# Kernel tuning notes

Measured on AMD Instinct MI355X. Metric: run time of the kernel, lower is better.

Reference implementation:

```python
import jax, jax.numpy as jnp
import numpy as np

B, S, HID = 2, 2048, 4096
H, KV, D = 32, 8, 128
ROPE_BASE = 10000.0
SCALE = 1.0 / (D ** 0.5)


def setup_inputs() -> dict:
    key = jax.random.key(0)
    k1, k2, k3 = jax.random.split(key, 3)
    hidden_states = jax.random.normal(k1, (B, S, HID), dtype=jnp.float32)
    position_ids = jnp.broadcast_to(jnp.arange(S, dtype=jnp.int32)[None, :], (B, S))
    Wqkv = jax.random.normal(k2, ((H + 2 * KV) * D, HID), dtype=jnp.float32) * (HID ** -0.5)
    Wo = jax.random.normal(k3, (HID, HID), dtype=jnp.float32) * (HID ** -0.5)
    return {"hidden_states": hidden_states, "position_ids": position_ids,
            "Wqkv": Wqkv, "Wo": Wo}


def _rotate_half(x):
    x1, x2 = jnp.split(x, 2, axis=-1)
    return jnp.concatenate([-x2, x1], axis=-1)


def _rope_cos_sin(position_ids):
    # inv_freq: [D/2]
    inv_freq = 1.0 / (ROPE_BASE ** (jnp.arange(0, D, 2, dtype=jnp.float32) / D))
    freqs = position_ids.astype(jnp.float32)[:, :, None] * inv_freq[None, None, :]  # [B,S,D/2]
    emb = jnp.concatenate([freqs, freqs], axis=-1)  # [B,S,D]
    # broadcast over heads: [B,1,S,D]
    return jnp.cos(emb)[:, None, :, :], jnp.sin(emb)[:, None, :, :]


def reference(hidden_states, position_ids, Wqkv, Wo):
    # fused QKV projection (no bias)
    qkv = jnp.einsum('bsh,oh->bso', hidden_states, Wqkv)  # [B,S,(H+2KV)*D]
    q, k, v = jnp.split(qkv, [H * D, (H + KV) * D], axis=-1)
    q = q.reshape(B, S, H, D).transpose(0, 2, 1, 3)    # [B,H,S,D]
    k = k.reshape(B, S, KV, D).transpose(0, 2, 1, 3)   # [B,KV,S,D]
    v = v.reshape(B, S, KV, D).transpose(0, 2, 1, 3)   # [B,KV,S,D]

    cos, sin = _rope_cos_sin(position_ids)
    q = q * cos + _rotate_half(q) * sin
    k = k * cos + _rotate_half(k) * sin

    # GQA: repeat_interleave kv heads to match q heads
    rep = H // KV
    k_full = jnp.repeat(k, rep, axis=1)  # [B,H,S,D]
    v_full = jnp.repeat(v, rep, axis=1)

    scores = jnp.einsum('bhqd,bhkd->bhqk', q, k_full) * SCALE  # [B,H,S,S]
    causal = jnp.tril(jnp.ones((S, S), dtype=bool))
    scores = jnp.where(causal[None, None, :, :], scores, jnp.float32(-jnp.inf))
    attn = jax.nn.softmax(scores, axis=-1)
    out = jnp.einsum('bhqk,bhkd->bhqd', attn, v_full)  # [B,H,S,D]
    out = out.transpose(0, 2, 1, 3).reshape(B, S, H * D)
    return jnp.einsum('bso,ho->bsh', out, Wo)  # o_proj, Wo is [out,in]
```

## Files before the change

kernel.cpp:

```cpp
#include <hip/hip_runtime.h>
#include <stdint.h>
#include <stddef.h>

#define Bsz   2
#define Ssz   2048
#define HIDsz 4096
#define Hsz   32
#define KVsz  8
#define Dsz   128
#define NQKV  6144
#define QSCALE 0.12752057463f
#define L2_1E4_64 0.20762050595f

typedef __bf16 bf16x8 __attribute__((ext_vector_type(8)));
typedef __bf16 bf16x2 __attribute__((ext_vector_type(2)));
typedef float  f32x4  __attribute__((ext_vector_type(4)));
typedef float  f32x16 __attribute__((ext_vector_type(16)));
typedef unsigned short u16;
typedef u16 u16x4 __attribute__((ext_vector_type(4)));
typedef u16 u16x8 __attribute__((ext_vector_type(8)));
typedef uint32_t u32x4 __attribute__((ext_vector_type(4)));

__device__ __forceinline__ u16 f2bf(float f) {
  uint32_t u = __builtin_bit_cast(uint32_t, f);
  u = (u + 0x7FFFu + ((u >> 16) & 1u)) >> 16;
  return (u16)u;
}
__device__ __forceinline__ float bf2f(u16 h) {
  return __builtin_bit_cast(float, (uint32_t)h << 16);
}
__device__ __forceinline__ uint32_t packc(float lo, float hi_) {
  bf16x2 t;
  t[0] = (__bf16)lo; t[1] = (__bf16)hi_;
  return __builtin_bit_cast(uint32_t, t);
}

#define GLDS(gp, lp) __builtin_amdgcn_global_load_lds( \
    (__attribute__((address_space(1))) void*)(void*)(gp), \
    (__attribute__((address_space(3))) void*)(lp), 16, 0, 0)

#define N4_HS  ((Bsz * Ssz * HIDsz) / 4)
#define N4_WQ  ((NQKV * HIDsz) / 4)
#define N4_WO  ((HIDsz * HIDsz) / 4)
__global__ __launch_bounds__(256) void k_cvt3(const float* __restrict__ hs,
                                              const float* __restrict__ wqkv,
                                              const float* __restrict__ wo,
                                              u16* __restrict__ xbf,
                                              u16* __restrict__ wqbf,
                                              u16* __restrict__ wobf) {
  int i = blockIdx.x * 256 + threadIdx.x;
  const float* src; u16* dst; int off;
  if (i < N4_HS)                   { src = hs;   dst = xbf;  off = i; }
  else if (i < N4_HS + N4_WQ)      { src = wqkv; dst = wqbf; off = i - N4_HS; }
  else if (i < N4_HS + N4_WQ + N4_WO) { src = wo; dst = wobf; off = i - N4_HS - N4_WQ; }
  else return;
  float4 v = ((const float4*)src)[off];
  u16x4 o;
  o.x = f2bf(v.x); o.y = f2bf(v.y); o.z = f2bf(v.z); o.w = f2bf(v.w);
  ((u16x4*)dst)[off] = o;
}


#define BARX do { asm volatile("" ::: "memory"); __builtin_amdgcn_s_barrier(); \
                  asm volatile("" ::: "memory"); } while (0)
#define VM6  asm volatile("s_waitcnt vmcnt(6)" ::: "memory")
#define VM0  asm volatile("s_waitcnt vmcnt(0)" ::: "memory")

#define LOADA4(P_, Q_, F_) do {                                               \
    afr[F_][0] = LDA(P_, Q_, 0, 0); afr[F_][1] = LDA(P_, Q_, 0, 1);           \
    afr[F_][2] = LDA(P_, Q_, 1, 0); afr[F_][3] = LDA(P_, Q_, 1, 1);           \
  } while (0)

#define LOADB8(P_) do {                                                       \
    _Pragma("unroll") for (int nf = 0; nf < 4; ++nf) {                        \
      bfr[nf][0] = LDB(P_, nf, 0); bfr[nf][1] = LDB(P_, nf, 1); }             \
  } while (0)

#define MMA16(Q_, F_) do {                                                    \
    __builtin_amdgcn_s_setprio(1);                                            \
    _Pragma("unroll") for (int nf = 0; nf < 4; ++nf) {                        \
      acc[(Q_)*2][nf]   = __builtin_amdgcn_mfma_f32_16x16x32_bf16(afr[F_][0], bfr[nf][0], acc[(Q_)*2][nf],   0,0,0); \
      acc[(Q_)*2+1][nf] = __builtin_amdgcn_mfma_f32_16x16x32_bf16(afr[F_][2], bfr[nf][0], acc[(Q_)*2+1][nf], 0,0,0); \
    }                                                                         \
    _Pragma("unroll") for (int nf = 0; nf < 4; ++nf) {                        \
      acc[(Q_)*2][nf]   = __builtin_amdgcn_mfma_f32_16x16x32_bf16(afr[F_][1], bfr[nf][1], acc[(Q_)*2][nf],   0,0,0); \
      acc[(Q_)*2+1][nf] = __builtin_amdgcn_mfma_f32_16x16x32_bf16(afr[F_][3], bfr[nf][1], acc[(Q_)*2+1][nf], 0,0,0); \
    }                                                                         \
    __builtin_amdgcn_s_setprio(0);                                            \
  } while (0)

#define TLS 258

template <int MODE>
__global__ __launch_bounds__(512, 1) void k_gemm256(const u16* __restrict__ A,
                                                    const u16* __restrict__ Bm,
                                                    float* __restrict__ Cv,
                                                    const int* __restrict__ pos,
                                                    u16* __restrict__ Qr,
                                                    int M, int N, int K_ld,
                                                    int K_len) {
  constexpr int LDS_BYTES = (MODE == 1) ? (256 * TLS * 2) : (4 * 256 * 64 * 2);
  __shared__ __align__(16) char LDSBUF[LDS_BYTES];
  u16* SA0 = (u16*)LDSBUF;
  u16* SB0 = (u16*)(LDSBUF + 65536);
  const int tid = threadIdx.x;
  const int w = tid >> 6, lane = tid & 63;
  const int g = lane >> 4, t = lane & 15;
  const int wr = w >> 2, wc = w & 3;
  const int cpx = gridDim.x >> 3;
  const int swz = (blockIdx.x & 7) * cpx + (blockIdx.x >> 3);

  int bm, bn;
  const u16 *Au = A, *Bu = Bm;
  float* Cu = Cv;
  if constexpr (MODE == 2) {
    const int t2 = swz & 127, h2 = swz >> 7;
    bm = t2 & 15; bn = 16 + (t2 >> 4);
    Au = A + h2 * 2048; Bu = Bm + h2 * 2048;
    Cu = Cv + (size_t)h2 * 4096 * 2048;
  } else {
    const int MBt = M >> 8;
    bm = swz % MBt; bn = swz / MBt;
  }
  const int m0 = bm << 8, n0 = bn << 8;

  const char* Ab = (const char*)Au;
  const char* Bb = (const char*)Bu;
  const size_t rowK = (size_t)K_ld * 2;
  const int srcx = ((lane & 7) ^ (lane >> 3)) << 4;
  const int l3 = lane >> 3;
  const int tx = (t & 7) << 4;

  auto SToff = [&](int h, int j) -> int {
    int ii = w * 2 + j;
    return (ii < 8) ? (h * 64 + ii * 8) : (128 + h * 64 + (ii - 8) * 8);
  };
  auto STAGE_A = [&](int p, int T, int h) {
#pragma unroll
    for (int j = 0; j < 2; ++j) {
      int rb = SToff(h, j);
      GLDS(Ab + (size_t)(m0 + rb + l3) * rowK + (size_t)T * 128 + srcx,
           &SA0[p * 16384 + rb * 64]);
    }
  };
  auto STAGE_B = [&](int p, int T, int h) {
#pragma unroll
    for (int j = 0; j < 2; ++j) {
      int rb = SToff(h, j);
      GLDS(Bb + (size_t)(n0 + rb + l3) * rowK + (size_t)T * 128 + srcx,
           &SB0[p * 16384 + rb * 64]);
    }
  };
  auto LDA = [&](int p, int q, int fr, int kk) -> bf16x8 {
    int ar = wr * 128 + q * 32 + fr * 16 + t;
    const char* ptr = (const char*)&SA0[p * 16384] + ar * 128 + ((kk * 64 + 16 * g) ^ tx);
    return __builtin_bit_cast(bf16x8, *(const u16x8*)ptr);
  };
  auto LDB = [&](int p, int nf, int kk) -> bf16x8 {
    int br = wc * 64 + nf * 16 + t;
    const char* ptr = (const char*)&SB0[p * 16384] + br * 128 + ((kk * 64 + 16 * g) ^ tx);
    return __builtin_bit_cast(bf16x8, *(const u16x8*)ptr);
  };

  f32x4 acc[8][4];
#pragma unroll
  for (int i = 0; i < 8; ++i)
#pragma unroll
    for (int j = 0; j < 4; ++j) acc[i][j] = (f32x4){0.f, 0.f, 0.f, 0.f};
  bf16x8 bfr[4][2];
  bf16x8 afr[2][4];

  STAGE_A(0, 0, 0); STAGE_B(0, 0, 0); STAGE_A(0, 0, 1); STAGE_B(0, 0, 1);
  STAGE_A(1, 1, 0); STAGE_B(1, 1, 0); STAGE_B(1, 1, 1);
  VM6;
  __builtin_amdgcn_s_barrier();

  const int NI = (K_len >> 7) - 1;
  for (int i = 0; i < NI; ++i) {
    const int T1 = 2 * i + 1, T2 = 2 * i + 2, T3 = 2 * i + 3;
    LOADB8(0); LOADA4(0, 0, 0);
    STAGE_A(1, T1, 1); LOADA4(0, 1, 1); MMA16(0, 0); BARX;
    STAGE_B(0, T2, 0); LOADA4(0, 2, 0); MMA16(1, 1); BARX;
    STAGE_B(0, T2, 1); LOADA4(0, 3, 1); MMA16(2, 0); BARX;
    STAGE_A(0, T2, 0); MMA16(3, 1); VM6; BARX;
    LOADB8(1); LOADA4(1, 0, 0);
    STAGE_A(0, T2, 1); LOADA4(1, 1, 1); MMA16(0, 0); BARX;
    STAGE_B(1, T3, 0); LOADA4(1, 2, 0); MMA16(1, 1); BARX;
    STAGE_A(1, T3, 0); LOADA4(1, 3, 1); MMA16(2, 0); BARX;
    STAGE_B(1, T3, 1); MMA16(3, 1); VM6; BARX;
  }
  {
    const int TL_ = (K_len >> 6) - 1;
    LOADB8(0); LOADA4(0, 0, 0);
    STAGE_A(1, TL_, 1); LOADA4(0, 1, 1); MMA16(0, 0); BARX;
    LOADA4(0, 2, 0); MMA16(1, 1); BARX;
    LOADA4(0, 3, 1); MMA16(2, 0); BARX;
    MMA16(3, 1); VM0; BARX;
    LOADB8(1); LOADA4(1, 0, 0);
    LOADA4(1, 1, 1); MMA16(0, 0); BARX;
    LOADA4(1, 2, 0); MMA16(1, 1); BARX;
    LOADA4(1, 3, 1); MMA16(2, 0); BARX;
    MMA16(3, 1);
  }

  if constexpr (MODE == 0 || MODE == 2) {
    const int cstride = (MODE == 0) ? N : 2048;
    const int cbase   = (MODE == 0) ? n0 : (n0 - 4096);
#pragma unroll
    for (int fi = 0; fi < 8; ++fi)
#pragma unroll
      for (int nf = 0; nf < 4; ++nf)
#pragma unroll
        for (int r = 0; r < 4; ++r) {
          int row = m0 + wr * 128 + fi * 16 + 4 * g + r;
          int col = cbase + wc * 64 + nf * 16 + t;
          Cu[(size_t)row * cstride + col] = acc[fi][nf][r];
        }
  } else {
    u16* TL = (u16*)LDSBUF;
    __syncthreads();
#pragma unroll
    for (int fi = 0; fi < 8; ++fi)
#pragma unroll
      for (int nf = 0; nf < 4; ++nf)
#pragma unroll
        for (int r = 0; r < 4; ++r)
          TL[(wr * 128 + fi * 16 + 4 * g + r) * TLS + wc * 64 + nf * 16 + t] =
              f2bf(acc[fi][nf][r]);
    __syncthreads();

    const int j = lane;
    const float ifr = exp2f(-(float)j * L2_1E4_64);
#pragma unroll 1
    for (int it = 0; it < 64; ++it) {
      int combo = w * 64 + it;
      int row = combo & 255;
      int hh = combo >> 8;
      int tok = m0 + row;
      int b = tok >> 11, s = tok & (Ssz - 1);
      float x1 = bf2f(TL[row * TLS + hh * 128 + j]);
      float x2 = bf2f(TL[row * TLS + hh * 128 + 64 + j]);
      float p = (float)pos[tok];
      float ang = p * ifr;
      float sn, cs;
      __sincosf(ang, &sn, &cs);
      float o1 = (x1 * cs - x2 * sn) * QSCALE;
      float o2 = (x2 * cs + x1 * sn) * QSCALE;
      int h = (n0 >> 7) + hh;
      u16* o = Qr + ((size_t)(b * Hsz + h) * Ssz + s) * Dsz;
      o[j] = f2bf(o1); o[j + 64] = f2bf(o2);
    }
  }
}

__global__ __launch_bounds__(256) void k_ropeK2(const float* __restrict__ Cp,
                                                const int* __restrict__ pos,
                                                u16* __restrict__ Kr) {
  int idx = blockIdx.x * 256 + threadIdx.x;
  if (idx >= Bsz * Ssz * KVsz * 64) return;
  const size_t OFF2 = (size_t)4096 * 2048;
  int j = idx & 63;
  int kvh = (idx >> 6) & 7;
  int bs = idx >> 9;
  size_t p0 = (size_t)bs * 2048 + kvh * 128 + j;
  float x1 = Cp[p0] + Cp[p0 + OFF2];
  float x2 = Cp[p0 + 64] + Cp[p0 + 64 + OFF2];
  float p = (float)pos[bs];
  float ang = p * exp2f(-(float)j * L2_1E4_64);
  float sn, cs;
  __sincosf(ang, &sn, &cs);
  int b = bs >> 11, sidx = bs & (Ssz - 1);
  u16* o = Kr + ((size_t)(b * KVsz + kvh) * Ssz + sidx) * Dsz;
  o[j] = f2bf(x1 * cs - x2 * sn);
  o[j + 64] = f2bf(x2 * cs + x1 * sn);
}

__global__ __launch_bounds__(256) void k_vtrans2(const float* __restrict__ Cp,
                                                 u16* __restrict__ Vt) {
  __shared__ __align__(16) u16 Tl[64 * 72];
  const int tid = threadIdx.x;
  const int bk = blockIdx.y;
  const int s0 = (blockIdx.x >> 1) * 64;
  const int d0 = (blockIdx.x & 1) * 64;
  const int b = bk >> 3, kvh = bk & 7;
  const size_t OFF2 = (size_t)4096 * 2048;
  const size_t base = (size_t)(b * Ssz + s0) * 2048 + 1024 + kvh * 128 + d0;
#pragma unroll
  for (int p = 0; p < 2; ++p) {
    int cid = p * 256 + tid;
    int r = cid >> 3, co = cid & 7;
    int chunk = co ^ ((r >> 3) & 7);
    const float* s1 = Cp + base + (size_t)r * 2048 + co * 8;
    u16x8 v;
#pragma unroll
    for (int e = 0; e < 8; ++e) v[e] = f2bf(s1[e] + s1[OFF2 + e]);
    *(u16x8*)((char*)Tl + r * 144 + chunk * 16) = v;
  }
  __syncthreads();
#pragma unroll
  for (int p = 0; p < 2; ++p) {
    int cid = p * 256 + tid;
    int dr = cid >> 3, c = cid & 7;
    u16x8 v;
#pragma unroll
    for (int j = 0; j < 8; ++j) {
      int s = 8 * c + j;
      v[j] = *(const u16*)((char*)Tl + s * 144 + (((dr >> 3) ^ c) * 16) + (dr & 7) * 2);
    }
    *(u16x8*)(Vt + ((size_t)bk * Dsz + d0 + dr) * Ssz + s0 + 8 * c) = v;
  }
}

__global__ __launch_bounds__(512, 1) void k_attn(const u16* __restrict__ Qr,
                                                 const u16* __restrict__ Kr,
                                                 const u16* __restrict__ Vt,
                                                 u16* __restrict__ AO) {
  __shared__ __align__(16) u16 Kl[2][64 * 128];
  __shared__ __align__(16) u16 Vl[2][128 * 64];
  const int tid = threadIdx.x;
  const int w = tid >> 6, lane = tid & 63;
  const int q = lane & 31, hi = lane >> 5;
  const int bh = blockIdx.y;
  const int b = bh >> 5, h = bh & 31;
  const int kvh = h >> 2;
  const int bx = blockIdx.x;

  const int xq = (q & 7) << 4;
  int koff[8][2], voff[4][4];
#pragma unroll
  for (int ds = 0; ds < 8; ++ds) {
    int c = (ds * 32 + hi * 16) ^ xq;
    koff[ds][0] = q * 256 + c;
    koff[ds][1] = (32 + q) * 256 + c;
  }
#pragma unroll
  for (int ks = 0; ks < 4; ++ks) {
    int c = (ks * 32 + hi * 16) ^ xq;
#pragma unroll
    for (int dt = 0; dt < 4; ++dt)
      voff[ks][dt] = (dt * 32 + q) * 128 + c;
  }

  const char* Kbase = (const char*)(Kr + (size_t)(b * KVsz + kvh) * Ssz * Dsz);
  const char* Vbase = (const char*)(Vt + (size_t)(b * KVsz + kvh) * Dsz * Ssz);

  auto STAGE = [&](int bu, int kt2) {
    const char* Kb = Kbase + (size_t)kt2 * (64 * 256);
    const char* Vb = Vbase + (size_t)kt2 * 128;
#pragma unroll
    for (int j = 0; j < 2; ++j) {
      int flat = j * 512 + tid;
      int row = flat >> 4, colb = ((flat & 15) * 16) ^ ((row & 7) << 4);
      GLDS(Kb + (size_t)row * 256 + colb, (char*)&Kl[bu][0] + flat * 16);
    }
#pragma unroll
    for (int j = 0; j < 2; ++j) {
      int flat = j * 512 + tid;
      int row = flat >> 3, colb = ((flat & 7) * 16) ^ ((row & 7) << 4);
      GLDS(Vb + (size_t)row * (Ssz * 2) + colb, (char*)&Vl[bu][0] + flat * 16);
    }
  };

#pragma unroll 1
  for (int pass = 0; pass < 2; ++pass) {
    const int bxr = pass ? bx : (7 - bx);
    const int q0 = bxr * 256;
    const int qw = q0 + w * 32;
    const int ntiles = 4 * bxr + 4;
    const int qg = qw + q;

    const u16* Qb = Qr + ((size_t)bh * Ssz + qw + q) * Dsz + hi * 8;
    bf16x8 qf[8];
#pragma unroll
    for (int ds = 0; ds < 8; ++ds)
      qf[ds] = __builtin_bit_cast(bf16x8, *(const u16x8*)(Qb + ds * 16));

    f32x16 oacc[4];
#pragma unroll
    for (int dt = 0; dt < 4; ++dt)
#pragma unroll
      for (int r = 0; r < 16; ++r) oacc[dt][r] = 0.f;
    float mr = -1e30f, lr = 0.f;

    STAGE(0, 0);
    __syncthreads();

    auto TILE = [&](int bufc, int kt) {
      const int k0 = kt * 64;
      if (kt + 1 < ntiles) STAGE(bufc ^ 1, kt + 1);

      if (k0 <= qw + 31) {
        const char* Kb = (const char*)&Kl[bufc][0];
        const char* Vb = (const char*)&Vl[bufc][0];
        f32x16 pa0, pa1;
#pragma unroll
        for (int r = 0; r < 16; ++r) { pa0[r] = 0.f; pa1[r] = 0.f; }
        __builtin_amdgcn_s_setprio(1);
#pragma unroll
        for (int ds = 0; ds < 8; ++ds) {
          bf16x8 kf0 = __builtin_bit_cast(bf16x8, *(const u16x8*)(Kb + koff[ds][0]));
          pa0 = __builtin_amdgcn_mfma_f32_32x32x16_bf16(kf0, qf[ds], pa0, 0, 0, 0);
          bf16x8 kf1 = __builtin_bit_cast(bf16x8, *(const u16x8*)(Kb + koff[ds][1]));
          pa1 = __builtin_amdgcn_mfma_f32_32x32x16_bf16(kf1, qf[ds], pa1, 0, 0, 0);
        }
        __builtin_amdgcn_s_setprio(0);

        if (k0 + 63 > qw) {
#pragma unroll
          for (int reg = 0; reg < 16; ++reg) {
            const int kb = (reg & 3) + 8 * (reg >> 2) + 4 * hi;
            if (k0 + kb > qg)      pa0[reg] = -1e30f;
            if (k0 + 32 + kb > qg) pa1[reg] = -1e30f;
          }
        }
        float tmx[16];
#pragma unroll
        for (int i = 0; i < 16; ++i) tmx[i] = fmaxf(pa0[i], pa1[i]);
#pragma unroll
        for (int s = 8; s > 0; s >>= 1)
#pragma unroll
          for (int i = 0; i < s; ++i) tmx[i] = fmaxf(tmx[i], tmx[i + s]);
        const float mx = fmaxf(tmx[0], __shfl_xor(tmx[0], 32, 64));
        if (!__all(mx <= mr + 4.0f)) {
          const float mnew = fmaxf(mr, mx);
          const float corr = exp2f(mr - mnew);
          lr *= corr;
#pragma unroll
          for (int dt = 0; dt < 4; ++dt)
#pragma unroll
            for (int reg = 0; reg < 16; ++reg) oacc[dt][reg] *= corr;
          mr = mnew;
        }
        float su[16];
#pragma unroll
        for (int reg = 0; reg < 16; ++reg) {
          pa0[reg] = exp2f(pa0[reg] - mr);
          pa1[reg] = exp2f(pa1[reg] - mr);
          su[reg] = pa0[reg] + pa1[reg];
        }
#pragma unroll
        for (int s = 8; s > 0; s >>= 1)
#pragma unroll
          for (int i = 0; i < s; ++i) su[i] += su[i + s];
        lr += su[0] + __shfl_xor(su[0], 32, 64);

        uint32_t W0[4][2], W1[4][2];
#pragma unroll
        for (int r2 = 0; r2 < 4; ++r2)
#pragma unroll
          for (int c = 0; c < 2; ++c) {
            W0[r2][c] = packc(pa0[4 * r2 + 2 * c], pa0[4 * r2 + 2 * c + 1]);
            W1[r2][c] = packc(pa1[4 * r2 + 2 * c], pa1[4 * r2 + 2 * c + 1]);
          }

        __builtin_amdgcn_s_setprio(1);
#pragma unroll
        for (int ks = 0; ks < 4; ++ks) {
          const int T = ks >> 1, r2e = 2 * (ks & 1);
          uint32_t a0 = T ? W1[r2e][0]     : W0[r2e][0];
          uint32_t a1 = T ? W1[r2e][1]     : W0[r2e][1];
          uint32_t b0 = T ? W1[r2e + 1][0] : W0[r2e + 1][0];
          uint32_t b1 = T ? W1[r2e + 1][1] : W0[r2e + 1][1];
          asm("v_permlane32_swap_b32 %0, %1" : "+v"(a0), "+v"(b0));
          asm("v_permlane32_swap_b32 %0, %1" : "+v"(a1), "+v"(b1));
          u32x4 fw; fw[0] = a0; fw[1] = a1; fw[2] = b0; fw[3] = b1;
          bf16x8 pf = __builtin_bit_cast(bf16x8, fw);
#pragma unroll
          for (int dt = 0; dt < 4; ++dt) {
            bf16x8 vf = __builtin_bit_cast(bf16x8, *(const u16x8*)(Vb + voff[ks][dt]));
            oacc[dt] = __builtin_amdgcn_mfma_f32_32x32x16_bf16(vf, pf, oacc[dt], 0, 0, 0);
          }
        }
        __builtin_amdgcn_s_setprio(0);
      }
      __syncthreads();
    };

    for (int kt = 0; kt < ntiles; kt += 2) {
      TILE(0, kt);
      TILE(1, kt + 1);
    }

    const float inv = 1.f / lr;
    u16* Ob = AO + ((size_t)(b * Ssz) + qw + q) * HIDsz + h * Dsz + hi * 4;
#pragma unroll
    for (int dt = 0; dt < 4; ++dt)
#pragma unroll
      for (int r2 = 0; r2 < 4; ++r2) {
        u16x4 o4;
#pragma unroll
        for (int j = 0; j < 4; ++j) o4[j] = f2bf(oacc[dt][4 * r2 + j] * inv);
        *(u16x4*)(Ob + dt * 32 + r2 * 8) = o4;
      }
  }
}

extern "C" void kernel_launch(void* const* d_in, const int* in_sizes, int n_in,
                              void* d_out, int out_size, void* d_ws, size_t ws_size,
                              hipStream_t stream) {
  (void)in_sizes; (void)n_in; (void)out_size;
  const float* hs   = (const float*)d_in[0];
  const int*   pos  = (const int*)d_in[1];
  const float* Wqkv = (const float*)d_in[2];
  const float* Wo   = (const float*)d_in[3];

  char* ws = (char*)d_ws;
  const size_t SZ_XBF = (size_t)4096 * 4096 * 2;
  const size_t SZ_WQ  = (size_t)6144 * 4096 * 2;
  const size_t SZ_WO  = (size_t)4096 * 4096 * 2;
  const size_t SZ_QR  = (size_t)Bsz * Hsz * Ssz * Dsz * 2;
  const size_t SZ_KR  = (size_t)Bsz * KVsz * Ssz * Dsz * 2;
  const size_t SZ_VT  = SZ_KR;

  size_t off = 0;
  u16*   Xbf   = (u16*)(ws + off);  off += SZ_XBF;
  u16*   Wq_bf = (u16*)(ws + off);  off += SZ_WQ;
  u16*   Wo_bf = (u16*)(ws + off);  off += SZ_WO;
  u16*   Qr    = (u16*)(ws + off);  off += SZ_QR;
  u16*   Kr    = (u16*)(ws + off);  off += SZ_KR;
  u16*   Vt    = (u16*)(ws + off);  off += SZ_VT;
  u16*   AO    = Xbf;
  float* Cp    = (float*)d_out;
  if (ws_size < off) return;

  k_cvt3<<<(N4_HS + N4_WQ + N4_WO + 255) / 256, 256, 0, stream>>>(
      hs, Wqkv, Wo, Xbf, Wq_bf, Wo_bf);

  k_gemm256<1><<<256, 512, 0, stream>>>(Xbf, Wq_bf, nullptr, pos, Qr,
                                        Bsz * Ssz, NQKV, HIDsz, HIDsz);

  k_gemm256<2><<<256, 512, 0, stream>>>(Xbf, Wq_bf, Cp, nullptr, nullptr,
                                        Bsz * Ssz, NQKV, HIDsz, 2048);

  k_ropeK2<<<(Bsz * Ssz * KVsz * 64) / 256, 256, 0, stream>>>(Cp, pos, Kr);
  k_vtrans2<<<dim3(64, Bsz * KVsz), 256, 0, stream>>>(Cp, Vt);

  k_attn<<<dim3(4, Bsz * Hsz), 512, 0, stream>>>(Qr, Kr, Vt, AO);

  k_gemm256<0><<<256, 512, 0, stream>>>(AO, Wo_bf, (float*)d_out, nullptr,
                                        nullptr, Bsz * Ssz, HIDsz, HIDsz, HIDsz);
}
```

Before: 464.1 us.

## Triple-buffer K/V tiles in attention with vmcnt-based partial waits

```diff
diff --git a/kernel.cpp b/kernel.cpp
--- a/kernel.cpp
+++ b/kernel.cpp
@@ -315,8 +315,8 @@
                                                  const u16* __restrict__ Kr,
                                                  const u16* __restrict__ Vt,
                                                  u16* __restrict__ AO) {
-  __shared__ __align__(16) u16 Kl[2][64 * 128];
-  __shared__ __align__(16) u16 Vl[2][128 * 64];
+  __shared__ __align__(16) u16 Kl[3][64 * 128];
+  __shared__ __align__(16) u16 Vl[3][128 * 64];
   const int tid = threadIdx.x;
   const int w = tid >> 6, lane = tid & 63;
   const int q = lane & 31, hi = lane >> 5;
@@ -383,15 +383,22 @@
     float mr = -1e30f, lr = 0.f;
 
     STAGE(0, 0);
-    __syncthreads();
-
-    auto TILE = [&](int bufc, int kt) {
+    STAGE(1, 1);
+    asm volatile("s_waitcnt vmcnt(4)" ::: "memory");
+    __builtin_amdgcn_s_barrier();
+    asm volatile("" ::: "memory");
+
+    int bc = 0, sc = 2;
+#pragma unroll 1
+    for (int kt = 0; kt < ntiles; ++kt) {
+      if (kt + 2 < ntiles) {
+        STAGE(sc, kt + 2);
+        sc = (sc == 2) ? 0 : sc + 1;
+      }
       const int k0 = kt * 64;
-      if (kt + 1 < ntiles) STAGE(bufc ^ 1, kt + 1);
-
       if (k0 <= qw + 31) {
-        const char* Kb = (const char*)&Kl[bufc][0];
-        const char* Vb = (const char*)&Vl[bufc][0];
+        const char* Kb = (const char*)&Kl[bc][0];
+        const char* Vb = (const char*)&Vl[bc][0];
         f32x16 pa0, pa1;
 #pragma unroll
         for (int r = 0; r < 16; ++r) { pa0[r] = 0.f; pa1[r] = 0.f; }
@@ -473,13 +480,16 @@
         }
         __builtin_amdgcn_s_setprio(0);
       }
-      __syncthreads();
-    };
-
-    for (int kt = 0; kt < ntiles; kt += 2) {
-      TILE(0, kt);
-      TILE(1, kt + 1);
-    }
+      if (kt + 1 < ntiles) {
+        asm volatile("" ::: "memory");
+        if (kt + 2 < ntiles) asm volatile("s_waitcnt vmcnt(4)" ::: "memory");
+        else                 asm volatile("s_waitcnt vmcnt(0)" ::: "memory");
+        __builtin_amdgcn_s_barrier();
+        asm volatile("" ::: "memory");
+      }
+      bc = (bc == 2) ? 0 : bc + 1;
+    }
+    __syncthreads();
 
     const float inv = 1.f / lr;
     u16* Ob = AO + ((size_t)(b * Ssz) + qw + q) * HIDsz + h * Dsz + hi * 4;
```

Measured after the change: 473.8 us. 1.02x slower.
